# Kernel tuning notes

Measured on AMD Instinct MI355X. Metric: run time of the kernel, lower is better.

The kernel has to match this reference:

```python
import jax, jax.numpy as jnp
import numpy as np

NFFT = 64
P = 8
L_CP = 8
HID = 128


def setup_inputs() -> dict:
    key = jax.random.key(0)
    ks = jax.random.split(key, 8)
    B = 131072
    Y = jax.random.normal(ks[0], (B, NFFT, 2), dtype=jnp.float32)
    # unit-magnitude pilot symbols (QPSK-like) so LS division is well-conditioned
    phase = jax.random.uniform(ks[1], (B, P), dtype=jnp.float32) * (2.0 * np.pi)
    Xp = jnp.stack([jnp.cos(phase), jnp.sin(phase)], axis=-1)  # [B,P,2]
    # comb pilots spanning [0, NFFT-1] (sorted; extrapolation branches inactive)
    pilot_pos = jnp.array([0, 9, 18, 27, 36, 45, 54, 63], dtype=jnp.int32)
    s = 0.05
    W1 = jax.random.normal(ks[2], (64, HID), dtype=jnp.float32) * s
    b1 = jnp.zeros((HID,), jnp.float32)
    W2 = jax.random.normal(ks[3], (HID, HID), dtype=jnp.float32) * s
    b2 = jnp.zeros((HID,), jnp.float32)
    W3 = jax.random.normal(ks[4], (HID, 64), dtype=jnp.float32) * s
    b3 = jnp.zeros((64,), jnp.float32)
    est_w = jnp.ones((1,), jnp.float32)
    alpha = jnp.float32(0.5)
    # softplus^{-1}(0.5) as in torch init
    decay_param = jnp.float32(np.log(np.exp(0.5) - 1.0))
    window_logits = jnp.zeros((L_CP,), jnp.float32)
    return dict(Y=Y, Xp=Xp, pilot_pos=pilot_pos, W1=W1, b1=b1, W2=W2, b2=b2,
                W3=W3, b3=b3, est_w=est_w, alpha=alpha,
                decay_param=decay_param, window_logits=window_logits)


def reference(Y, Xp, pilot_pos, W1, b1, W2, b2, W3, b3, est_w, alpha,
              decay_param, window_logits):
    B = Y.shape[0]
    # ---- LS estimate at pilot bins: LS[k] = Y[pilot_pos[k]] / Xp[k] ----
    Yp = jnp.take(Y, pilot_pos, axis=1)              # [B,P,2]
    a, b = Yp[..., 0], Yp[..., 1]
    c, d = Xp[..., 0], Xp[..., 1]
    den = c * c + d * d
    ls_r = (a * c + b * d) / den                     # [B,P]
    ls_i = (b * c - a * d) / den
    w0 = est_w[0]
    wls_r, wls_i = ls_r * w0, ls_i * w0
    # ---- pilot-processor MLP (P<=32 branch) ----
    # torch: stack([real,imag],-1).flatten() -> interleaved r0,i0,r1,i1,...
    ls_in = jnp.stack([ls_r, ls_i], axis=-1).reshape(B, 2 * P)  # [B,16]
    ls_in = jnp.pad(ls_in, ((0, 0), (0, 64 - 2 * P)))           # pad to 64
    h = jax.nn.relu(ls_in @ W1 + b1)
    h = jax.nn.relu(h @ W2 + b2)
    o = jnp.tanh(h @ W3 + b3)                         # [B,64]
    nn_r, nn_i = o[:, :P], o[:, P:2 * P]
    al = jnp.clip(alpha, 0.0, 1.0)
    comb_r = al * wls_r + (1.0 - al) * nn_r          # [B,P]
    comb_i = al * wls_i + (1.0 - al) * nn_i
    # ---- distance-aware interpolation (vectorized over all Nfft bins) ----
    # pilot_pos_1based = pos+1 then -1 inside interpolate cancels -> 0-based locs
    pilot_loc = pilot_pos.astype(jnp.float32)        # [P], spans 0..NFFT-1
    i = jnp.arange(NFFT, dtype=jnp.float32)          # [N]
    left = jnp.clip(jnp.searchsorted(pilot_loc, i, side='right') - 1, 0, P - 2)
    right = left + 1
    x0, x1 = pilot_loc[left], pilot_loc[right]       # [N]
    decay = jax.nn.softplus(decay_param)
    w_l = jnp.exp(-decay * jnp.abs(i - x0))          # [N]
    w_r = jnp.exp(-decay * jnp.abs(x1 - i))
    w_s = w_l + w_r + 1e-12
    H_r = (w_l * comb_r[:, left] + w_r * comb_r[:, right]) / w_s  # [B,N]
    H_i = (w_l * comb_i[:, left] + w_r * comb_i[:, right]) / w_s
    # ---- DFT denoise: ifft, window first L_cp taps, zero rest, fft ----
    H = jax.lax.complex(H_r, H_i)                    # [B,N] complex64
    h_time = jnp.fft.ifft(H, axis=-1)
    window = jax.nn.sigmoid(window_logits).astype(jnp.complex64)  # [L_CP]
    h_win = jnp.concatenate([h_time[:, :L_CP] * window,
                             jnp.zeros_like(h_time[:, L_CP:])], axis=-1)
    H_hat = jnp.fft.fft(h_win, axis=-1)
    return jnp.stack([jnp.real(H_hat), jnp.imag(H_hat)], axis=-1)  # [B,N,2]
```

## Files before the change

### kernel.cpp

```cpp
#include <hip/hip_runtime.h>
#include <hip/hip_bf16.h>
#include <math.h>

typedef __attribute__((ext_vector_type(8))) short short8v;
typedef __attribute__((ext_vector_type(4))) float f32x4;

__device__ __forceinline__ unsigned short f2bf(float x) {
    union { float f; unsigned u; } v; v.f = x;
    unsigned r = v.u + 0x7FFF + ((v.u >> 16) & 1);
    return (unsigned short)(r >> 16);
}
__device__ __forceinline__ unsigned cvtpk(float a, float b) {
    unsigned short lo = __builtin_bit_cast(unsigned short, __float2bfloat16(a));
    unsigned short hi = __builtin_bit_cast(unsigned short, __float2bfloat16(b));
    return (unsigned)lo | ((unsigned)hi << 16);
}
__device__ __forceinline__ float fast_tanh(float x) {
    float e = __expf(2.0f * x);
    return 1.0f - 2.0f / (e + 1.0f);
}
__device__ __host__ __forceinline__ int sigma_perm(int ct, int p) {
    return 32 * (ct >> 1) + 8 * (p >> 2) + 4 * (ct & 1) + (p & 3);
}

#define WS_TAB  4096
#define T_W1    0
#define T_W2    5120
#define T_W3    22528
#define T_MP    24704
#define T_SH    29824

__global__ __launch_bounds__(256) void ce_prep_kernel(
    const int* __restrict__ pilot_pos,
    const float* __restrict__ decay_param,
    const float* __restrict__ window_logits,
    const float* __restrict__ W1, const float* __restrict__ W2,
    const float* __restrict__ W3,
    char* __restrict__ ws)
{
    unsigned short* tab = (unsigned short*)(ws + WS_TAB);
    int t = threadIdx.x;
    if (blockIdx.x != 0) {
        int i = (int)(blockIdx.x - 1) * 256 + t;
        int row = i >> 7, k = i & 127;
        int ct = row >> 4, p = row & 15;
        tab[T_W2 + row * 136 + k] = f2bf(W2[k * 128 + sigma_perm(ct, p)]);
        return;
    }
    __shared__ float win[8], Gr[64], Gi[64], wln[64], wrn[64];
    __shared__ int lefts[64], pos[8];
    __shared__ float sA[64 * 16];
    if (t < 8) {
        pos[t] = pilot_pos[t];
        win[t] = 1.0f / (1.0f + expf(-window_logits[t]));
    }
    __syncthreads();
    float decay = log1pf(expf(decay_param[0]));
    if (t < 64) {
        float gr = 0.f, gi = 0.f;
        #pragma unroll
        for (int n = 0; n < 8; ++n) {
            float ang = 6.283185307179586f * (float)(n * t) * (1.0f / 64.0f);
            gr += win[n] * cosf(ang);
            gi += win[n] * sinf(ang);
        }
        Gr[t] = gr * (1.0f / 64.0f);
        Gi[t] = gi * (1.0f / 64.0f);
        int lft = 0;
        #pragma unroll
        for (int p = 1; p < 8; ++p) if (pos[p] <= t) lft = p;
        if (lft > 6) lft = 6;
        float x0 = (float)pos[lft], x1 = (float)pos[lft + 1], fi = (float)t;
        float wl = expf(-decay * fabsf(fi - x0));
        float wr = expf(-decay * fabsf(x1 - fi));
        float wsum = wl + wr + 1e-12f;
        lefts[t] = lft; wln[t] = wl / wsum; wrn[t] = wr / wsum;
    }
    __syncthreads();
    if (t < 64) {
        float ar[8], ai[8];
        for (int p = 0; p < 8; ++p) { ar[p] = 0.f; ai[p] = 0.f; }
        for (int i = 0; i < 64; ++i) {
            int d = (i - t) & 63;
            float gr = Gr[d], gi = Gi[d];
            int lft = lefts[i];
            float wa = wln[i], wb = wrn[i];
            ar[lft]     += wa * gr;  ai[lft]     += wa * gi;
            ar[lft + 1] += wb * gr;  ai[lft + 1] += wb * gi;
        }
        for (int p = 0; p < 8; ++p) {
            sA[t * 16 + 2 * p]     = ar[p];
            sA[t * 16 + 2 * p + 1] = ai[p];
        }
    }
    __syncthreads();
    for (int i = t; i < 128 * 32; i += 256) {
        int row = i >> 5, k = i & 31;
        unsigned short v = 0;
        if (k < 16) {
            int j = row, mm = j >> 1, s = j & 1;
            int ct = row >> 4; (void)ct;
            int p = k >> 1, u = k & 1;
            float Ar = sA[mm * 16 + 2 * p], Ai = sA[mm * 16 + 2 * p + 1];
            float val = (s == 0) ? ((u == 0) ? Ar : -Ai)
                                 : ((u == 0) ? Ai :  Ar);
            v = f2bf(val);
        }
        tab[T_MP + row * 40 + k] = v;
    }
    for (int i = t; i < 128 * 32; i += 256) {
        int row = i >> 5, k = i & 31;
        int ct = row >> 4, p = row & 15;
        tab[T_W1 + row * 40 + k] =
            (k < 16) ? f2bf(W1[k * 128 + sigma_perm(ct, p)]) : (unsigned short)0;
    }
    for (int i = t; i < 16 * 128; i += 256) {
        int col = i >> 7, k = i & 127;
        tab[T_W3 + col * 136 + k] = f2bf(W3[k * 64 + col]);
    }
}

__global__ __launch_bounds__(512) void ce_fused(
    const float* __restrict__ Y, const float* __restrict__ Xp,
    const int* __restrict__ pilot_pos,
    const float* __restrict__ b1, const float* __restrict__ b2,
    const float* __restrict__ b3,
    const float* __restrict__ est_w, const float* __restrict__ alpha,
    const char* __restrict__ ws,
    float* __restrict__ out, int B)
{
    __shared__ unsigned short sT[T_SH];

    const int t = threadIdx.x;
    const int w = t >> 6, l = t & 63;
    const int m = l & 15, kg = l >> 4;
    const long e = (long)blockIdx.x * 128 + w * 16 + m;
    const long ec = (e < B) ? e : (long)(B - 1);

    typedef union { unsigned u[4]; short8v v; } pk_t;
    const f32x4 z4 = {0.f, 0.f, 0.f, 0.f};

    float2 y0, y1, y2, y3;
    float4 x0, x1;
    const bool act = (kg < 2);
    if (act) {
        const float* yrow = Y + ec * 128;
        const float4* xr = (const float4*)(Xp + ec * 16 + kg * 8);
        int p0 = kg * 4;
        y0 = *(const float2*)(yrow + pilot_pos[p0 + 0] * 2);
        y1 = *(const float2*)(yrow + pilot_pos[p0 + 1] * 2);
        y2 = *(const float2*)(yrow + pilot_pos[p0 + 2] * 2);
        y3 = *(const float2*)(yrow + pilot_pos[p0 + 3] * 2);
        x0 = xr[0]; x1 = xr[1];
    }

    {
        const uint4* src = (const uint4*)(ws + WS_TAB);
        uint4* dst = (uint4*)sT;
        for (int i = t; i < T_SH / 8; i += 512) dst[i] = src[i];
    }

    float lsv[8];
    short8v xb = {0, 0, 0, 0, 0, 0, 0, 0};
    if (act) {
        float inv;
        inv = 1.0f / (x0.x * x0.x + x0.y * x0.y);
        lsv[0] = (y0.x * x0.x + y0.y * x0.y) * inv;
        lsv[1] = (y0.y * x0.x - y0.x * x0.y) * inv;
        inv = 1.0f / (x0.z * x0.z + x0.w * x0.w);
        lsv[2] = (y1.x * x0.z + y1.y * x0.w) * inv;
        lsv[3] = (y1.y * x0.z - y1.x * x0.w) * inv;
        inv = 1.0f / (x1.x * x1.x + x1.y * x1.y);
        lsv[4] = (y2.x * x1.x + y2.y * x1.y) * inv;
        lsv[5] = (y2.y * x1.x - y2.x * x1.y) * inv;
        inv = 1.0f / (x1.z * x1.z + x1.w * x1.w);
        lsv[6] = (y3.x * x1.z + y3.y * x1.w) * inv;
        lsv[7] = (y3.y * x1.z - y3.x * x1.w) * inv;
        pk_t px;
        px.u[0] = cvtpk(lsv[0], lsv[1]);
        px.u[1] = cvtpk(lsv[2], lsv[3]);
        px.u[2] = cvtpk(lsv[4], lsv[5]);
        px.u[3] = cvtpk(lsv[6], lsv[7]);
        xb = px.v;
    }
    __syncthreads();

    pk_t h1[4];
    #pragma unroll
    for (int ks = 0; ks < 4; ++ks) {
        #pragma unroll
        for (int half = 0; half < 2; ++half) {
            int ct = 2 * ks + half;
            float4 bv = *(const float4*)(b1 + ks * 32 + kg * 8 + half * 4);
            f32x4 cin = { bv.x, bv.y, bv.z, bv.w };
            short8v wf = *(const short8v*)(sT + T_W1 + (ct * 16 + m) * 40 + kg * 8);
            f32x4 acc = __builtin_amdgcn_mfma_f32_16x16x32_bf16(wf, xb, cin, 0, 0, 0);
            h1[ks].u[2 * half]     = cvtpk(fmaxf(acc[0], 0.f), fmaxf(acc[1], 0.f));
            h1[ks].u[2 * half + 1] = cvtpk(fmaxf(acc[2], 0.f), fmaxf(acc[3], 0.f));
        }
    }

    f32x4 a2[8];
    #pragma unroll
    for (int ct = 0; ct < 8; ++ct) {
        float4 bv = *(const float4*)(b2 + 32 * (ct >> 1) + 8 * kg + 4 * (ct & 1));
        f32x4 cin = { bv.x, bv.y, bv.z, bv.w };
        a2[ct] = cin;
    }
    #pragma unroll
    for (int ks = 0; ks < 4; ++ks) {
        short8v hf = h1[ks].v;
        #pragma unroll
        for (int ct = 0; ct < 8; ++ct) {
            short8v wf = *(const short8v*)(sT + T_W2 + (ct * 16 + m) * 136 + ks * 32 + kg * 8);
            a2[ct] = __builtin_amdgcn_mfma_f32_16x16x32_bf16(wf, hf, a2[ct], 0, 0, 0);
        }
    }

    pk_t h2[4];
    #pragma unroll
    for (int ks = 0; ks < 4; ++ks) {
        #pragma unroll
        for (int half = 0; half < 2; ++half) {
            int ct = 2 * ks + half;
            h2[ks].u[2 * half]     = cvtpk(fmaxf(a2[ct][0], 0.f), fmaxf(a2[ct][1], 0.f));
            h2[ks].u[2 * half + 1] = cvtpk(fmaxf(a2[ct][2], 0.f), fmaxf(a2[ct][3], 0.f));
        }
    }

    float4 b3c = *(const float4*)(b3 + 4 * kg);
    f32x4 acc3 = { b3c.x, b3c.y, b3c.z, b3c.w };
    #pragma unroll
    for (int ks = 0; ks < 4; ++ks) {
        short8v wf = *(const short8v*)(sT + T_W3 + m * 136 + ks * 32 + kg * 8);
        acc3 = __builtin_amdgcn_mfma_f32_16x16x32_bf16(wf, h2[ks].v, acc3, 0, 0, 0);
    }

    pk_t myv;
    myv.u[0] = 0; myv.u[1] = 0; myv.u[2] = 0; myv.u[3] = 0;
    {
        float o0 = __shfl_down(acc3[0], 32);
        float o1 = __shfl_down(acc3[1], 32);
        float o2 = __shfl_down(acc3[2], 32);
        float o3 = __shfl_down(acc3[3], 32);
        float w0 = est_w[0];
        float al = fminf(fmaxf(alpha[0], 0.f), 1.f);
        float oma = 1.0f - al;
        if (act) {
            float olo[4] = { acc3[0], acc3[1], acc3[2], acc3[3] };
            float ohi[4] = { o0, o1, o2, o3 };
            #pragma unroll
            for (int r = 0; r < 4; ++r) {
                float cr = al * (lsv[2 * r] * w0)     + oma * fast_tanh(olo[r]);
                float ci = al * (lsv[2 * r + 1] * w0) + oma * fast_tanh(ohi[r]);
                myv.u[r] = cvtpk(cr, ci);
            }
        }
    }
    short8v vb = myv.v;

    if (e < B) {
        float* orow = out + e * 128;
        f32x4 eacc[8];
        #pragma unroll
        for (int ct = 0; ct < 8; ++ct) {
            short8v mf = *(const short8v*)(sT + T_MP + (ct * 16 + m) * 40 + kg * 8);
            eacc[ct] = __builtin_amdgcn_mfma_f32_16x16x32_bf16(mf, vb, z4, 0, 0, 0);
        }
        #pragma unroll
        for (int ct = 0; ct < 8; ++ct) {
            float4 st = { eacc[ct][0], eacc[ct][1], eacc[ct][2], eacc[ct][3] };
            *(float4*)(orow + ct * 16 + kg * 4) = st;
        }
    }
}

extern "C" void kernel_launch(void* const* d_in, const int* in_sizes, int n_in,
                              void* d_out, int out_size, void* d_ws, size_t ws_size,
                              hipStream_t stream) {
    const float* Y             = (const float*)d_in[0];
    const float* Xp            = (const float*)d_in[1];
    const int*   pilot_pos     = (const int*)d_in[2];
    const float* W1            = (const float*)d_in[3];
    const float* b1            = (const float*)d_in[4];
    const float* W2            = (const float*)d_in[5];
    const float* b2            = (const float*)d_in[6];
    const float* W3            = (const float*)d_in[7];
    const float* b3            = (const float*)d_in[8];
    const float* est_w         = (const float*)d_in[9];
    const float* alpha         = (const float*)d_in[10];
    const float* decay_param   = (const float*)d_in[11];
    const float* window_logits = (const float*)d_in[12];
    float* out = (float*)d_out;
    char* ws = (char*)d_ws;

    int B = in_sizes[0] / 128;

    hipLaunchKernelGGL(ce_prep_kernel, dim3(65), dim3(256), 0, stream,
                       pilot_pos, decay_param, window_logits, W1, W2, W3, ws);
    int grid = (B + 127) / 128;
    hipLaunchKernelGGL(ce_fused, dim3(grid), dim3(512), 0, stream,
                       Y, Xp, pilot_pos, b1, b2, b3, est_w, alpha,
                       ws, out, B);
}
```

Measured before the change: 58.80 us.

## Make fused kernel persistent with grid-stride loop and prefetch of next group's pilots

Caps the grid at 512 blocks and loops each block over groups of 128 batch elements. The shared-memory weight table is loaded once per block instead of once per group, and the pilot loads for the next group are issued before the current group's MLP runs. The aim is to amortize the table copy and hide global-load latency, at the cost of fewer resident blocks and a serialized per-block loop.

```diff
diff --git a/kernel.cpp b/kernel.cpp
--- a/kernel.cpp
+++ b/kernel.cpp
@@ -98,8 +98,7 @@
         int row = i >> 5, k = i & 31;
         unsigned short v = 0;
         if (k < 16) {
-            int j = row, mm = j >> 1, s = j & 1;
-            int ct = row >> 4; (void)ct;
+            int mm = row >> 1, s = row & 1;
             int p = k >> 1, u = k & 1;
             float Ar = sA[mm * 16 + 2 * p], Ai = sA[mm * 16 + 2 * p + 1];
             float val = (s == 0) ? ((u == 0) ? Ar : -Ai)
@@ -127,30 +126,41 @@
     const float* __restrict__ b3,
     const float* __restrict__ est_w, const float* __restrict__ alpha,
     const char* __restrict__ ws,
-    float* __restrict__ out, int B)
+    float* __restrict__ out, int B, int ngroups)
 {
     __shared__ unsigned short sT[T_SH];
 
     const int t = threadIdx.x;
     const int w = t >> 6, l = t & 63;
     const int m = l & 15, kg = l >> 4;
-    const long e = (long)blockIdx.x * 128 + w * 16 + m;
-    const long ec = (e < B) ? e : (long)(B - 1);
+    const bool act = (kg < 2);
+    const int eoff = w * 16 + m;
 
     typedef union { unsigned u[4]; short8v v; } pk_t;
     const f32x4 z4 = {0.f, 0.f, 0.f, 0.f};
 
+    int pp0 = 0, pp1 = 0, pp2 = 0, pp3 = 0;
+    if (act) {
+        int p0 = kg * 4;
+        pp0 = pilot_pos[p0 + 0] * 2;
+        pp1 = pilot_pos[p0 + 1] * 2;
+        pp2 = pilot_pos[p0 + 2] * 2;
+        pp3 = pilot_pos[p0 + 3] * 2;
+    }
+
+    long g = blockIdx.x;
+
     float2 y0, y1, y2, y3;
     float4 x0, x1;
-    const bool act = (kg < 2);
-    if (act) {
+    if (act && g < ngroups) {
+        long e = g * 128 + eoff;
+        long ec = (e < B) ? e : (long)(B - 1);
         const float* yrow = Y + ec * 128;
         const float4* xr = (const float4*)(Xp + ec * 16 + kg * 8);
-        int p0 = kg * 4;
-        y0 = *(const float2*)(yrow + pilot_pos[p0 + 0] * 2);
-        y1 = *(const float2*)(yrow + pilot_pos[p0 + 1] * 2);
-        y2 = *(const float2*)(yrow + pilot_pos[p0 + 2] * 2);
-        y3 = *(const float2*)(yrow + pilot_pos[p0 + 3] * 2);
+        y0 = *(const float2*)(yrow + pp0);
+        y1 = *(const float2*)(yrow + pp1);
+        y2 = *(const float2*)(yrow + pp2);
+        y3 = *(const float2*)(yrow + pp3);
         x0 = xr[0]; x1 = xr[1];
     }
 
@@ -159,118 +169,135 @@
         uint4* dst = (uint4*)sT;
         for (int i = t; i < T_SH / 8; i += 512) dst[i] = src[i];
     }
-
-    float lsv[8];
-    short8v xb = {0, 0, 0, 0, 0, 0, 0, 0};
-    if (act) {
-        float inv;
-        inv = 1.0f / (x0.x * x0.x + x0.y * x0.y);
-        lsv[0] = (y0.x * x0.x + y0.y * x0.y) * inv;
-        lsv[1] = (y0.y * x0.x - y0.x * x0.y) * inv;
-        inv = 1.0f / (x0.z * x0.z + x0.w * x0.w);
-        lsv[2] = (y1.x * x0.z + y1.y * x0.w) * inv;
-        lsv[3] = (y1.y * x0.z - y1.x * x0.w) * inv;
-        inv = 1.0f / (x1.x * x1.x + x1.y * x1.y);
-        lsv[4] = (y2.x * x1.x + y2.y * x1.y) * inv;
-        lsv[5] = (y2.y * x1.x - y2.x * x1.y) * inv;
-        inv = 1.0f / (x1.z * x1.z + x1.w * x1.w);
-        lsv[6] = (y3.x * x1.z + y3.y * x1.w) * inv;
-        lsv[7] = (y3.y * x1.z - y3.x * x1.w) * inv;
-        pk_t px;
-        px.u[0] = cvtpk(lsv[0], lsv[1]);
-        px.u[1] = cvtpk(lsv[2], lsv[3]);
-        px.u[2] = cvtpk(lsv[4], lsv[5]);
-        px.u[3] = cvtpk(lsv[6], lsv[7]);
-        xb = px.v;
-    }
     __syncthreads();
 
-    pk_t h1[4];
-    #pragma unroll
-    for (int ks = 0; ks < 4; ++ks) {
-        #pragma unroll
-        for (int half = 0; half < 2; ++half) {
-            int ct = 2 * ks + half;
-            float4 bv = *(const float4*)(b1 + ks * 32 + kg * 8 + half * 4);
+    const float w0 = est_w[0];
+    const float al = fminf(fmaxf(alpha[0], 0.f), 1.f);
+    const float oma = 1.0f - al;
+    const float4 b3c = *(const float4*)(b3 + 4 * kg);
+
+    for (; g < ngroups; g += gridDim.x) {
+        float lsv[8];
+        short8v xb = {0, 0, 0, 0, 0, 0, 0, 0};
+        if (act) {
+            float inv;
+            inv = 1.0f / (x0.x * x0.x + x0.y * x0.y);
+            lsv[0] = (y0.x * x0.x + y0.y * x0.y) * inv;
+            lsv[1] = (y0.y * x0.x - y0.x * x0.y) * inv;
+            inv = 1.0f / (x0.z * x0.z + x0.w * x0.w);
+            lsv[2] = (y1.x * x0.z + y1.y * x0.w) * inv;
+            lsv[3] = (y1.y * x0.z - y1.x * x0.w) * inv;
+            inv = 1.0f / (x1.x * x1.x + x1.y * x1.y);
+            lsv[4] = (y2.x * x1.x + y2.y * x1.y) * inv;
+            lsv[5] = (y2.y * x1.x - y2.x * x1.y) * inv;
+            inv = 1.0f / (x1.z * x1.z + x1.w * x1.w);
+            lsv[6] = (y3.x * x1.z + y3.y * x1.w) * inv;
+            lsv[7] = (y3.y * x1.z - y3.x * x1.w) * inv;
+            pk_t px;
+            px.u[0] = cvtpk(lsv[0], lsv[1]);
+            px.u[1] = cvtpk(lsv[2], lsv[3]);
+            px.u[2] = cvtpk(lsv[4], lsv[5]);
+            px.u[3] = cvtpk(lsv[6], lsv[7]);
+            xb = px.v;
+        }
+
+        long gn = g + gridDim.x;
+        if (act && gn < ngroups) {
+            long e = gn * 128 + eoff;
+            long ec = (e < B) ? e : (long)(B - 1);
+            const float* yrow = Y + ec * 128;
+            const float4* xr = (const float4*)(Xp + ec * 16 + kg * 8);
+            y0 = *(const float2*)(yrow + pp0);
+            y1 = *(const float2*)(yrow + pp1);
+            y2 = *(const float2*)(yrow + pp2);
+            y3 = *(const float2*)(yrow + pp3);
+            x0 = xr[0]; x1 = xr[1];
+        }
+
+        pk_t h1[4];
+        #pragma unroll
+        for (int ks = 0; ks < 4; ++ks) {
+            #pragma unroll
+            for (int half = 0; half < 2; ++half) {
+                int ct = 2 * ks + half;
+                float4 bv = *(const float4*)(b1 + ks * 32 + kg * 8 + half * 4);
+                f32x4 cin = { bv.x, bv.y, bv.z, bv.w };
+                short8v wf = *(const short8v*)(sT + T_W1 + (ct * 16 + m) * 40 + kg * 8);
+                f32x4 acc = __builtin_amdgcn_mfma_f32_16x16x32_bf16(wf, xb, cin, 0, 0, 0);
+                h1[ks].u[2 * half]     = cvtpk(fmaxf(acc[0], 0.f), fmaxf(acc[1], 0.f));
+                h1[ks].u[2 * half + 1] = cvtpk(fmaxf(acc[2], 0.f), fmaxf(acc[3], 0.f));
+            }
+        }
+
+        f32x4 a2[8];
+        #pragma unroll
+        for (int ct = 0; ct < 8; ++ct) {
+            float4 bv = *(const float4*)(b2 + 32 * (ct >> 1) + 8 * kg + 4 * (ct & 1));
             f32x4 cin = { bv.x, bv.y, bv.z, bv.w };
-            short8v wf = *(const short8v*)(sT + T_W1 + (ct * 16 + m) * 40 + kg * 8);
-            f32x4 acc = __builtin_amdgcn_mfma_f32_16x16x32_bf16(wf, xb, cin, 0, 0, 0);
-            h1[ks].u[2 * half]     = cvtpk(fmaxf(acc[0], 0.f), fmaxf(acc[1], 0.f));
-            h1[ks].u[2 * half + 1] = cvtpk(fmaxf(acc[2], 0.f), fmaxf(acc[3], 0.f));
-        }
-    }
-
-    f32x4 a2[8];
-    #pragma unroll
-    for (int ct = 0; ct < 8; ++ct) {
-        float4 bv = *(const float4*)(b2 + 32 * (ct >> 1) + 8 * kg + 4 * (ct & 1));
-        f32x4 cin = { bv.x, bv.y, bv.z, bv.w };
-        a2[ct] = cin;
-    }
-    #pragma unroll
-    for (int ks = 0; ks < 4; ++ks) {
-        short8v hf = h1[ks].v;
-        #pragma unroll
-        for (int ct = 0; ct < 8; ++ct) {
-            short8v wf = *(const short8v*)(sT + T_W2 + (ct * 16 + m) * 136 + ks * 32 + kg * 8);
-            a2[ct] = __builtin_amdgcn_mfma_f32_16x16x32_bf16(wf, hf, a2[ct], 0, 0, 0);
-        }
-    }
-
-    pk_t h2[4];
-    #pragma unroll
-    for (int ks = 0; ks < 4; ++ks) {
-        #pragma unroll
-        for (int half = 0; half < 2; ++half) {
-            int ct = 2 * ks + half;
-            h2[ks].u[2 * half]     = cvtpk(fmaxf(a2[ct][0], 0.f), fmaxf(a2[ct][1], 0.f));
-            h2[ks].u[2 * half + 1] = cvtpk(fmaxf(a2[ct][2], 0.f), fmaxf(a2[ct][3], 0.f));
-        }
-    }
-
-    float4 b3c = *(const float4*)(b3 + 4 * kg);
-    f32x4 acc3 = { b3c.x, b3c.y, b3c.z, b3c.w };
-    #pragma unroll
-    for (int ks = 0; ks < 4; ++ks) {
-        short8v wf = *(const short8v*)(sT + T_W3 + m * 136 + ks * 32 + kg * 8);
-        acc3 = __builtin_amdgcn_mfma_f32_16x16x32_bf16(wf, h2[ks].v, acc3, 0, 0, 0);
-    }
-
-    pk_t myv;
-    myv.u[0] = 0; myv.u[1] = 0; myv.u[2] = 0; myv.u[3] = 0;
-    {
-        float o0 = __shfl_down(acc3[0], 32);
-        float o1 = __shfl_down(acc3[1], 32);
-        float o2 = __shfl_down(acc3[2], 32);
-        float o3 = __shfl_down(acc3[3], 32);
-        float w0 = est_w[0];
-        float al = fminf(fmaxf(alpha[0], 0.f), 1.f);
-        float oma = 1.0f - al;
-        if (act) {
-            float olo[4] = { acc3[0], acc3[1], acc3[2], acc3[3] };
-            float ohi[4] = { o0, o1, o2, o3 };
-            #pragma unroll
-            for (int r = 0; r < 4; ++r) {
-                float cr = al * (lsv[2 * r] * w0)     + oma * fast_tanh(olo[r]);
-                float ci = al * (lsv[2 * r + 1] * w0) + oma * fast_tanh(ohi[r]);
-                myv.u[r] = cvtpk(cr, ci);
-            }
-        }
-    }
-    short8v vb = myv.v;
-
-    if (e < B) {
-        float* orow = out + e * 128;
-        f32x4 eacc[8];
-        #pragma unroll
-        for (int ct = 0; ct < 8; ++ct) {
-            short8v mf = *(const short8v*)(sT + T_MP + (ct * 16 + m) * 40 + kg * 8);
-            eacc[ct] = __builtin_amdgcn_mfma_f32_16x16x32_bf16(mf, vb, z4, 0, 0, 0);
-        }
-        #pragma unroll
-        for (int ct = 0; ct < 8; ++ct) {
-            float4 st = { eacc[ct][0], eacc[ct][1], eacc[ct][2], eacc[ct][3] };
-            *(float4*)(orow + ct * 16 + kg * 4) = st;
+            a2[ct] = cin;
+        }
+        #pragma unroll
+        for (int ks = 0; ks < 4; ++ks) {
+            short8v hf = h1[ks].v;
+            #pragma unroll
+            for (int ct = 0; ct < 8; ++ct) {
+                short8v wf = *(const short8v*)(sT + T_W2 + (ct * 16 + m) * 136 + ks * 32 + kg * 8);
+                a2[ct] = __builtin_amdgcn_mfma_f32_16x16x32_bf16(wf, hf, a2[ct], 0, 0, 0);
+            }
+        }
+
+        pk_t h2[4];
+        #pragma unroll
+        for (int ks = 0; ks < 4; ++ks) {
+            #pragma unroll
+            for (int half = 0; half < 2; ++half) {
+                int ct = 2 * ks + half;
+                h2[ks].u[2 * half]     = cvtpk(fmaxf(a2[ct][0], 0.f), fmaxf(a2[ct][1], 0.f));
+                h2[ks].u[2 * half + 1] = cvtpk(fmaxf(a2[ct][2], 0.f), fmaxf(a2[ct][3], 0.f));
+            }
+        }
+
+        f32x4 acc3 = { b3c.x, b3c.y, b3c.z, b3c.w };
+        #pragma unroll
+        for (int ks = 0; ks < 4; ++ks) {
+            short8v wf = *(const short8v*)(sT + T_W3 + m * 136 + ks * 32 + kg * 8);
+            acc3 = __builtin_amdgcn_mfma_f32_16x16x32_bf16(wf, h2[ks].v, acc3, 0, 0, 0);
+        }
+
+        pk_t myv;
+        myv.u[0] = 0; myv.u[1] = 0; myv.u[2] = 0; myv.u[3] = 0;
+        {
+            float o0 = __shfl_down(acc3[0], 32);
+            float o1 = __shfl_down(acc3[1], 32);
+            float o2 = __shfl_down(acc3[2], 32);
+            float o3 = __shfl_down(acc3[3], 32);
+            if (act) {
+                float olo[4] = { acc3[0], acc3[1], acc3[2], acc3[3] };
+                float ohi[4] = { o0, o1, o2, o3 };
+                #pragma unroll
+                for (int r = 0; r < 4; ++r) {
+                    float cr = al * (lsv[2 * r] * w0)     + oma * fast_tanh(olo[r]);
+                    float ci = al * (lsv[2 * r + 1] * w0) + oma * fast_tanh(ohi[r]);
+                    myv.u[r] = cvtpk(cr, ci);
+                }
+            }
+        }
+        short8v vb = myv.v;
+
+        long e = g * 128 + eoff;
+        if (e < B) {
+            float* orow = out + e * 128;
+            f32x4 eacc[8];
+            #pragma unroll
+            for (int ct = 0; ct < 8; ++ct) {
+                short8v mf = *(const short8v*)(sT + T_MP + (ct * 16 + m) * 40 + kg * 8);
+                eacc[ct] = __builtin_amdgcn_mfma_f32_16x16x32_bf16(mf, vb, z4, 0, 0, 0);
+            }
+            #pragma unroll
+            for (int ct = 0; ct < 8; ++ct) {
+                float4 st = { eacc[ct][0], eacc[ct][1], eacc[ct][2], eacc[ct][3] };
+                *(float4*)(orow + ct * 16 + kg * 4) = st;
+            }
         }
     }
 }
@@ -295,11 +322,12 @@
     char* ws = (char*)d_ws;
 
     int B = in_sizes[0] / 128;
+    int ngroups = (B + 127) / 128;
 
     hipLaunchKernelGGL(ce_prep_kernel, dim3(65), dim3(256), 0, stream,
                        pilot_pos, decay_param, window_logits, W1, W2, W3, ws);
-    int grid = (B + 127) / 128;
+    int grid = (ngroups < 512) ? ngroups : 512;
     hipLaunchKernelGGL(ce_fused, dim3(grid), dim3(512), 0, stream,
                        Y, Xp, pilot_pos, b1, b2, b3, est_w, alpha,
-                       ws, out, B);
-}
+                       ws, out, B, ngroups);
+}
```

Result: slower. 96.88 us (+64.8%).
